# Performance work log

Hardware: AMD Instinct MI355X
Metric: run time of the kernel (lower is better)

## Reference

```python
import jax, jax.numpy as jnp
import numpy as np

MIN_LEVEL, MAX_LEVEL = 2, 5

# pywt Wavelet('db4') analysis filters (dec_lo / dec_hi)
DEC_LO = np.array([-0.010597401784997278, 0.032883011666982945, 0.030841381835986965,
                   -0.18703481171888114, -0.02798376941698385, 0.6308807679295904,
                   0.7148465705525415, 0.23037781330885523])
DEC_HI = np.array([-0.23037781330885523, 0.7148465705525415, -0.6308807679295904,
                   -0.02798376941698385, 0.18703481171888114, 0.030841381835986965,
                   -0.032883011666982945, -0.010597401784997278])
# pytorch_wavelets time-reverses the filters and uses cross-correlation (F.conv),
# which is exactly what lax.conv_general_dilated computes.
H0 = jnp.asarray(DEC_LO[::-1].copy(), jnp.float32)
H1 = jnp.asarray(DEC_HI[::-1].copy(), jnp.float32)


def _afb1d(x):
    """One-level analysis filter bank, 'zero' padding mode (pytorch_wavelets afb1d).
    x: (N, 1, T) -> (lo, hi) each (N, 1, floor((T+L-1)/2))."""
    T = x.shape[-1]
    L = H0.shape[0]
    out = (T + L - 1) // 2          # pywt.dwt_coeff_len(T, L, 'zero')
    p = 2 * out - T                 # total pad; extra zero goes to the right if odd
    xp = jnp.pad(x, ((0, 0), (0, 0), (p // 2, p - p // 2)))
    k = jnp.stack([H0, H1])[:, None, :]          # (2, 1, L)
    lohi = jax.lax.conv_general_dilated(
        xp, k, window_strides=(2,), padding='VALID',
        dimension_numbers=('NCH', 'OIH', 'NCH'))
    return lohi[:, 0:1, :], lohi[:, 1:2, :]


def _decompose(x, levels):
    """Batched multi-level DWT cascade over all features at once; per-feature
    decomposition level selected afterwards via one-hot / masking (same math as
    the original per-feature Python loop)."""
    B, S, F = x.shape
    cur = jnp.transpose(x, (0, 2, 1)).reshape(B * F, 1, S)
    los, his = [], []
    for _ in range(MAX_LEVEL):
        lo, hi = _afb1d(cur)

        def to_bsf(a):
            # zero-pad coeffs up to seq_len, back to (B, S, F) layout
            a = jnp.pad(a, ((0, 0), (0, 0), (0, S - a.shape[-1])))
            return jnp.transpose(a.reshape(B, F, S), (0, 2, 1))

        los.append(to_bsf(lo))
        his.append(to_bsf(hi))
        cur = lo
    los = jnp.stack(los)   # (MAX_LEVEL, B, S, F) lowpass after level j+1
    his = jnp.stack(his)   # (MAX_LEVEL, B, S, F) detail at level j+1

    # approx for feature f = lowpass after `levels[f]` levels
    sel = jax.nn.one_hot(levels - 1, MAX_LEVEL, dtype=x.dtype)      # (F, MAX_LEVEL)
    approx = jnp.einsum('lbsf,fl->bsf', los, sel)
    # details[i] only populated for i < levels[f]
    mask = (jnp.arange(MAX_LEVEL)[:, None] < levels[None, :]).astype(x.dtype)  # (L, F)
    details = his * mask[:, None, None, :]
    high_freq = details.sum(axis=0)
    low_freq = approx
    return approx, details, high_freq, low_freq


def setup_inputs() -> dict:
    key = jax.random.key(0)
    k1, k2 = jax.random.split(key)
    x = jax.random.normal(k1, (32, 4096, 64), jnp.float32)
    complexity_scores = jax.random.uniform(k2, (64,), jnp.float32)
    return {"x": x, "complexity_scores": complexity_scores}


def reference(x, complexity_scores):
    # level_scaled = min_level + round(score * (max_level - min_level)); Python round
    # and jnp.round both use round-half-to-even.
    levels = MIN_LEVEL + jnp.round(
        complexity_scores * (MAX_LEVEL - MIN_LEVEL)).astype(jnp.int32)
    levels = jnp.clip(levels, MIN_LEVEL, MAX_LEVEL)   # (F,)
    return _decompose(x, levels)
```

## Files before the change

### kernel.cpp

```cpp
#include <hip/hip_runtime.h>


#define NB 32
#define NS 4096
#define NF 64
#define NF4 16
#define BSF (NB * NS * NF)

typedef float f4v __attribute__((ext_vector_type(4)));

__constant__ float c_h0[8] = {
     0.23037781330885523f,  0.7148465705525415f,   0.6308807679295904f,
    -0.02798376941698385f, -0.18703481171888114f,  0.030841381835986965f,
     0.032883011666982945f, -0.010597401784997278f};
__constant__ float c_h1[8] = {
    -0.010597401784997278f, -0.032883011666982945f, 0.030841381835986965f,
     0.18703481171888114f,  -0.02798376941698385f,  -0.6308807679295904f,
     0.7148465705525415f,   -0.23037781330885523f};

__device__ __forceinline__ void levels4(const float* __restrict__ scores, int f4,
                                        int lv[4]) {
    f4v s = ((const f4v*)scores)[f4];
#pragma unroll
    for (int c = 0; c < 4; ++c) {
        int l = 2 + (int)rintf(s[c] * 3.0f);
        lv[c] = min(5, max(2, l));
    }
}

__global__ __launch_bounds__(256) void wl_l1(
    const f4v* __restrict__ x, f4v* __restrict__ lo1, f4v* __restrict__ det1)
{
    int t = blockIdx.x * 256 + threadIdx.x;
    int f4 = t & 15;
    int r = t >> 4;
    int nq = r & 511;
    int b  = r >> 9;
    int n0 = nq * 4;

    const f4v z = {0.f, 0.f, 0.f, 0.f};
    const f4v* row = x + (size_t)b * NS * NF4 + f4;
    f4v v[14];
    int base = 2 * n0 - 3;
#pragma unroll
    for (int j = 0; j < 14; ++j) {
        int m = base + j;
        v[j] = ((unsigned)m < (unsigned)NS) ? row[(size_t)m * NF4] : z;
    }
    f4v* lp = lo1  + (size_t)(b * 2048 + n0) * NF4 + f4;
    f4v* dp = det1 + (size_t)(b * NS   + n0) * NF4 + f4;
#pragma unroll
    for (int k = 0; k < 4; ++k) {
        f4v l = z, h = z;
#pragma unroll
        for (int i = 0; i < 8; ++i) { l += c_h0[i] * v[2*k + i]; h += c_h1[i] * v[2*k + i]; }
        lp[k * NF4] = l;
        dp[k * NF4] = h;
    }
}

template <int TIN, int LEN, int J>
__device__ __forceinline__ void pyr_level(
    const f4v* __restrict__ src_base, f4v* __restrict__ lo_out,
    f4v* __restrict__ det, int b, int f4, int tn, const int lv[4])
{
    const f4v z = {0.f, 0.f, 0.f, 0.f};
    const f4v* src = src_base + (size_t)b * TIN * NF4 + f4;
#pragma unroll
    for (int k = 0; k < LEN / 64; ++k) {
        int n = tn + 64 * k;
        f4v l = z, h = z;
        int base = 2 * n - 3;
#pragma unroll
        for (int i = 0; i < 8; ++i) {
            int m = base + i;
            if ((unsigned)m < (unsigned)TIN) {
                f4v vv = src[(size_t)m * NF4];
                l += c_h0[i] * vv;  h += c_h1[i] * vv;
            }
        }
        if (J >= 3) {
#pragma unroll
            for (int c = 0; c < 4; ++c) if (lv[c] < J) h[c] = 0.f;
        }
        lo_out[(size_t)(b * LEN + n) * NF4 + f4] = l;
        det[(size_t)(b * NS + n) * NF4 + f4] = h;
    }
}

__global__ __launch_bounds__(256) void wl_pyr(
    const f4v* __restrict__ lo1, f4v* __restrict__ lo2, f4v* __restrict__ lo3,
    f4v* __restrict__ lo4, f4v* __restrict__ lo5,
    f4v* __restrict__ det2, f4v* __restrict__ det3, f4v* __restrict__ det4,
    f4v* __restrict__ det5, const float* __restrict__ scores)
{
    int b  = blockIdx.x >> 2;
    int q  = blockIdx.x & 3;
    int fl = threadIdx.x & 3;
    int tn = threadIdx.x >> 2;
    int f4 = q * 4 + fl;
    int lv[4];
    levels4(scores, f4, lv);

    pyr_level<2048, 1024, 2>(lo1, lo2, det2, b, f4, tn, lv);
    __syncthreads();
    pyr_level<1024,  512, 3>(lo2, lo3, det3, b, f4, tn, lv);
    __syncthreads();
    pyr_level< 512,  256, 4>(lo3, lo4, det4, b, f4, tn, lv);
    __syncthreads();
    pyr_level< 256,  128, 5>(lo4, lo5, det5, b, f4, tn, lv);
}

__global__ __launch_bounds__(256) void wl_out(
    const f4v* __restrict__ lo2, const f4v* __restrict__ lo3,
    const f4v* __restrict__ lo4, const f4v* __restrict__ lo5,
    f4v* __restrict__ out4, const float* __restrict__ scores)
{
    int t = blockIdx.x * 256 + threadIdx.x;
    int f4 = t & 15;
    int r = t >> 4;
    int n = r & (NS - 1);
    int b = r >> 12;
    int lv[4];
    levels4(scores, f4, lv);

    const f4v z = {0.f, 0.f, 0.f, 0.f};
    f4v* det1 = out4 + (size_t)1 * (BSF / 4);
    f4v* det2 = out4 + (size_t)2 * (BSF / 4);
    f4v* det3 = out4 + (size_t)3 * (BSF / 4);
    f4v* det4 = out4 + (size_t)4 * (BSF / 4);
    f4v* det5 = out4 + (size_t)5 * (BSF / 4);

    f4v c2 = (n < 1024) ? lo2[(size_t)(b * 1024 + n) * NF4 + f4] : z;
    f4v c3 = (n <  512) ? lo3[(size_t)(b *  512 + n) * NF4 + f4] : z;
    f4v c4 = (n <  256) ? lo4[(size_t)(b *  256 + n) * NF4 + f4] : z;
    f4v c5 = (n <  128) ? lo5[(size_t)(b *  128 + n) * NF4 + f4] : z;

    f4v av;
#pragma unroll
    for (int c = 0; c < 4; ++c)
        av[c] = (lv[c] == 2) ? c2[c] : (lv[c] == 3) ? c3[c]
              : (lv[c] == 4) ? c4[c] : c5[c];

    f4v acc = z;
    if (n < 2048) acc += det1[t];
    if (n < 1024) acc += det2[t];
    if (n <  512) acc += det3[t];
    if (n <  256) acc += det4[t];
    if (n <  128) acc += det5[t];

    __builtin_nontemporal_store(av,  out4 + t);
    __builtin_nontemporal_store(acc, out4 + (size_t)6 * (BSF / 4) + t);
    __builtin_nontemporal_store(av,  out4 + (size_t)7 * (BSF / 4) + t);
    if (n >= 2048) __builtin_nontemporal_store(z, det1 + t);
    if (n >= 1024) __builtin_nontemporal_store(z, det2 + t);
    if (n >=  512) __builtin_nontemporal_store(z, det3 + t);
    if (n >=  256) __builtin_nontemporal_store(z, det4 + t);
    if (n >=  128) __builtin_nontemporal_store(z, det5 + t);
}

extern "C" void kernel_launch(void* const* d_in, const int* in_sizes, int n_in,
                              void* d_out, int out_size, void* d_ws, size_t ws_size,
                              hipStream_t stream)
{
    const f4v* x        = (const f4v*)d_in[0];
    const float* scores = (const float*)d_in[1];
    f4v* out4 = (f4v*)d_out;

    f4v* lo1 = (f4v*)d_ws;
    f4v* lo2 = lo1 + (size_t)NB * 2048 * NF4;
    f4v* lo3 = lo2 + (size_t)NB * 1024 * NF4;
    f4v* lo4 = lo3 + (size_t)NB *  512 * NF4;
    f4v* lo5 = lo4 + (size_t)NB *  256 * NF4;

    f4v* det1 = out4 + (size_t)1 * (BSF / 4);
    f4v* det2 = out4 + (size_t)2 * (BSF / 4);
    f4v* det3 = out4 + (size_t)3 * (BSF / 4);
    f4v* det4 = out4 + (size_t)4 * (BSF / 4);
    f4v* det5 = out4 + (size_t)5 * (BSF / 4);

    dim3 block(256);
    wl_l1 <<<dim3(NB * 512 * NF4 / 256), block, 0, stream>>>(x, lo1, det1);
    wl_pyr<<<dim3(NB * 4),              block, 0, stream>>>(lo1, lo2, lo3, lo4, lo5,
                                                            det2, det3, det4, det5, scores);
    wl_out<<<dim3(BSF / 4 / 256),       block, 0, stream>>>(lo2, lo3, lo4, lo5,
                                                            out4, scores);
}
```

Baseline: 339.1 us.

## Split pyramid kernel into per-level grid-wide launches and fuse level 5 into output

Result: faster. 310.3 us (-8.5%).

```diff
diff --git a/kernel.cpp b/kernel.cpp
--- a/kernel.cpp
+++ b/kernel.cpp
@@ -59,62 +59,51 @@
     }
 }
 
-template <int TIN, int LEN, int J>
-__device__ __forceinline__ void pyr_level(
-    const f4v* __restrict__ src_base, f4v* __restrict__ lo_out,
-    f4v* __restrict__ det, int b, int f4, int tn, const int lv[4])
+template <int J, int TIN, int LOG2LEN>
+__global__ __launch_bounds__(256) void wl_lvl(
+    const f4v* __restrict__ in, f4v* __restrict__ lo_out,
+    f4v* __restrict__ det, const float* __restrict__ scores)
 {
+    constexpr int LEN = 1 << LOG2LEN;
+    int t = blockIdx.x * 256 + threadIdx.x;
+    int f4 = t & (NF4 - 1);
+    int r = t >> 4;
+    int np = r & (LEN / 2 - 1);
+    int b = r >> (LOG2LEN - 1);
+    int n0 = 2 * np;
+
+    const f4v* row = in + (size_t)b * TIN * NF4 + f4;
     const f4v z = {0.f, 0.f, 0.f, 0.f};
-    const f4v* src = src_base + (size_t)b * TIN * NF4 + f4;
+    f4v v[10];
+    int base = n0 * 2 - 3;
 #pragma unroll
-    for (int k = 0; k < LEN / 64; ++k) {
-        int n = tn + 64 * k;
-        f4v l = z, h = z;
-        int base = 2 * n - 3;
+    for (int j = 0; j < 10; ++j) {
+        int m = base + j;
+        v[j] = ((unsigned)m < (unsigned)TIN) ? row[(size_t)m * NF4] : z;
+    }
+    f4v lo0 = z, hi0 = z, lo1 = z, hi1 = z;
 #pragma unroll
-        for (int i = 0; i < 8; ++i) {
-            int m = base + i;
-            if ((unsigned)m < (unsigned)TIN) {
-                f4v vv = src[(size_t)m * NF4];
-                l += c_h0[i] * vv;  h += c_h1[i] * vv;
-            }
-        }
-        if (J >= 3) {
+    for (int i = 0; i < 8; ++i) {
+        lo0 += c_h0[i] * v[i];      hi0 += c_h1[i] * v[i];
+        lo1 += c_h0[i] * v[i + 2];  hi1 += c_h1[i] * v[i + 2];
+    }
+    if (J >= 3) {
+        int lv[4];
+        levels4(scores, f4, lv);
 #pragma unroll
-            for (int c = 0; c < 4; ++c) if (lv[c] < J) h[c] = 0.f;
-        }
-        lo_out[(size_t)(b * LEN + n) * NF4 + f4] = l;
-        det[(size_t)(b * NS + n) * NF4 + f4] = h;
+        for (int c = 0; c < 4; ++c)
+            if (lv[c] < J) { hi0[c] = 0.f; hi1[c] = 0.f; }
     }
+    f4v* lp = lo_out + (size_t)(b * LEN + n0) * NF4 + f4;
+    lp[0] = lo0;  lp[NF4] = lo1;
+    f4v* dp = det + (size_t)(b * NS + n0) * NF4 + f4;
+    dp[0] = hi0;  dp[NF4] = hi1;
 }
 
-__global__ __launch_bounds__(256) void wl_pyr(
-    const f4v* __restrict__ lo1, f4v* __restrict__ lo2, f4v* __restrict__ lo3,
-    f4v* __restrict__ lo4, f4v* __restrict__ lo5,
-    f4v* __restrict__ det2, f4v* __restrict__ det3, f4v* __restrict__ det4,
-    f4v* __restrict__ det5, const float* __restrict__ scores)
-{
-    int b  = blockIdx.x >> 2;
-    int q  = blockIdx.x & 3;
-    int fl = threadIdx.x & 3;
-    int tn = threadIdx.x >> 2;
-    int f4 = q * 4 + fl;
-    int lv[4];
-    levels4(scores, f4, lv);
-
-    pyr_level<2048, 1024, 2>(lo1, lo2, det2, b, f4, tn, lv);
-    __syncthreads();
-    pyr_level<1024,  512, 3>(lo2, lo3, det3, b, f4, tn, lv);
-    __syncthreads();
-    pyr_level< 512,  256, 4>(lo3, lo4, det4, b, f4, tn, lv);
-    __syncthreads();
-    pyr_level< 256,  128, 5>(lo4, lo5, det5, b, f4, tn, lv);
-}
-
-__global__ __launch_bounds__(256) void wl_out(
+__global__ __launch_bounds__(256) void wl_final(
     const f4v* __restrict__ lo2, const f4v* __restrict__ lo3,
-    const f4v* __restrict__ lo4, const f4v* __restrict__ lo5,
-    f4v* __restrict__ out4, const float* __restrict__ scores)
+    const f4v* __restrict__ lo4, f4v* __restrict__ out4,
+    const float* __restrict__ scores)
 {
     int t = blockIdx.x * 256 + threadIdx.x;
     int f4 = t & 15;
@@ -125,38 +114,51 @@
     levels4(scores, f4, lv);
 
     const f4v z = {0.f, 0.f, 0.f, 0.f};
+    f4v d5 = z, l5 = z;
+    if (n < 128) {
+        const f4v* row = lo4 + (size_t)b * 256 * NF4 + f4;
+        int base = 2 * n - 3;
+        f4v hi = z;
+#pragma unroll
+        for (int i = 0; i < 8; ++i) {
+            int m = base + i;
+            if ((unsigned)m < 256u) {
+                f4v vv = row[(size_t)m * NF4];
+                l5 += c_h0[i] * vv;  hi += c_h1[i] * vv;
+            }
+        }
+#pragma unroll
+        for (int c = 0; c < 4; ++c) d5[c] = (lv[c] >= 5) ? hi[c] : 0.f;
+    }
+
     f4v* det1 = out4 + (size_t)1 * (BSF / 4);
     f4v* det2 = out4 + (size_t)2 * (BSF / 4);
     f4v* det3 = out4 + (size_t)3 * (BSF / 4);
     f4v* det4 = out4 + (size_t)4 * (BSF / 4);
-    f4v* det5 = out4 + (size_t)5 * (BSF / 4);
 
     f4v c2 = (n < 1024) ? lo2[(size_t)(b * 1024 + n) * NF4 + f4] : z;
     f4v c3 = (n <  512) ? lo3[(size_t)(b *  512 + n) * NF4 + f4] : z;
     f4v c4 = (n <  256) ? lo4[(size_t)(b *  256 + n) * NF4 + f4] : z;
-    f4v c5 = (n <  128) ? lo5[(size_t)(b *  128 + n) * NF4 + f4] : z;
-
     f4v av;
 #pragma unroll
     for (int c = 0; c < 4; ++c)
         av[c] = (lv[c] == 2) ? c2[c] : (lv[c] == 3) ? c3[c]
-              : (lv[c] == 4) ? c4[c] : c5[c];
+              : (lv[c] == 4) ? c4[c] : l5[c];
 
-    f4v acc = z;
+    f4v acc = d5;
     if (n < 2048) acc += det1[t];
     if (n < 1024) acc += det2[t];
     if (n <  512) acc += det3[t];
     if (n <  256) acc += det4[t];
-    if (n <  128) acc += det5[t];
 
     __builtin_nontemporal_store(av,  out4 + t);
+    __builtin_nontemporal_store(d5,  out4 + (size_t)5 * (BSF / 4) + t);
     __builtin_nontemporal_store(acc, out4 + (size_t)6 * (BSF / 4) + t);
     __builtin_nontemporal_store(av,  out4 + (size_t)7 * (BSF / 4) + t);
     if (n >= 2048) __builtin_nontemporal_store(z, det1 + t);
     if (n >= 1024) __builtin_nontemporal_store(z, det2 + t);
     if (n >=  512) __builtin_nontemporal_store(z, det3 + t);
     if (n >=  256) __builtin_nontemporal_store(z, det4 + t);
-    if (n >=  128) __builtin_nontemporal_store(z, det5 + t);
 }
 
 extern "C" void kernel_launch(void* const* d_in, const int* in_sizes, int n_in,
@@ -171,18 +173,16 @@
     f4v* lo2 = lo1 + (size_t)NB * 2048 * NF4;
     f4v* lo3 = lo2 + (size_t)NB * 1024 * NF4;
     f4v* lo4 = lo3 + (size_t)NB *  512 * NF4;
-    f4v* lo5 = lo4 + (size_t)NB *  256 * NF4;
 
     f4v* det1 = out4 + (size_t)1 * (BSF / 4);
     f4v* det2 = out4 + (size_t)2 * (BSF / 4);
     f4v* det3 = out4 + (size_t)3 * (BSF / 4);
     f4v* det4 = out4 + (size_t)4 * (BSF / 4);
-    f4v* det5 = out4 + (size_t)5 * (BSF / 4);
 
     dim3 block(256);
-    wl_l1 <<<dim3(NB * 512 * NF4 / 256), block, 0, stream>>>(x, lo1, det1);
-    wl_pyr<<<dim3(NB * 4),              block, 0, stream>>>(lo1, lo2, lo3, lo4, lo5,
-                                                            det2, det3, det4, det5, scores);
-    wl_out<<<dim3(BSF / 4 / 256),       block, 0, stream>>>(lo2, lo3, lo4, lo5,
-                                                            out4, scores);
+    wl_l1<<<dim3(NB * 512 * NF4 / 256), block, 0, stream>>>(x, lo1, det1);
+    wl_lvl<2, 2048, 10><<<dim3(NB * 512 * NF4 / 256), block, 0, stream>>>(lo1, lo2, det2, scores);
+    wl_lvl<3, 1024,  9><<<dim3(NB * 256 * NF4 / 256), block, 0, stream>>>(lo2, lo3, det3, scores);
+    wl_lvl<4,  512,  8><<<dim3(NB * 128 * NF4 / 256), block, 0, stream>>>(lo3, lo4, det4, scores);
+    wl_final<<<dim3(BSF / 4 / 256), block, 0, stream>>>(lo2, lo3, lo4, out4, scores);
 }
```
